# Performance work log

Measured on AMD Instinct MI355X. Metric: run time of the kernel, lower is better.

The kernel has to match this reference:

```python
import jax, jax.numpy as jnp
import numpy as np
from jax import lax

H = 64      # hidden_size
VOC = 512   # num_embedding
L = 2       # num_layers


def layernorm(x, g, b, eps=1e-5):
    mu = jnp.mean(x, axis=-1, keepdims=True)
    var = jnp.mean((x - mu) ** 2, axis=-1, keepdims=True)
    return (x - mu) * lax.rsqrt(var + eps) * g + b


def conv3d(x, w, b):
    # x: [B, U, V, W, Cin] (channels-last), w: [3,3,3,Cin,Cout]
    return lax.conv_general_dilated(
        x, w, (1, 1, 1), 'SAME',
        dimension_numbers=('NDHWC', 'DHWIO', 'NDHWC')) + b


def setup_inputs() -> dict:
    key = jax.random.key(0)
    ks = jax.random.split(key, 8)
    f = lambda k, s, sc: jax.random.normal(k, s, jnp.float32) * sc
    return {
        'code': jax.random.randint(ks[0], (2, 5, 1, 8, 8, 8), 0, VOC),
        'ncode': jax.random.randint(ks[1], (2, 3, 1, 8, 8, 8), 0, VOC),
        'emb': f(ks[2], (VOC, H), 0.02),
        'win': f(ks[3], (L, 3, 3, 3, H, 4 * H), 0.05),
        'bin_': jnp.zeros((L, 4 * H), jnp.float32),
        'gin_w': jnp.ones((L, 4 * H), jnp.float32),
        'gin_b': jnp.zeros((L, 4 * H), jnp.float32),
        'wh': f(ks[4], (L, 3, 3, 3, H, 4 * H), 0.05),
        'bh': jnp.zeros((L, 4 * H), jnp.float32),
        'gh_w': jnp.ones((L, 4 * H), jnp.float32),
        'gh_b': jnp.zeros((L, 4 * H), jnp.float32),
        'w1': f(ks[5], (H, H), 0.05),
        'b1': jnp.zeros((H,), jnp.float32),
        'ln_g': jnp.ones((H,), jnp.float32),
        'ln_b': jnp.zeros((H,), jnp.float32),
        'w2': f(ks[6], (H, VOC), 0.05),
        'b2': jnp.zeros((VOC,), jnp.float32),
    }


def _forward(code, ncode, emb, win, bin_, gin_w, gin_b, wh, bh, gh_w, gh_b,
             w1, b1, ln_g, ln_b, w2, b2):
    N, Sn, C, U, V, W = ncode.shape
    x = jnp.concatenate([code, ncode[:, :-1]], axis=1)  # [N,S,C,U,V,W]
    S = x.shape[1]
    x = jnp.transpose(x, (0, 2, 1, 3, 4, 5)).reshape(N * C, S, U, V, W)
    h = emb[x]  # [NC, S, U, V, W, H]
    Hd = h.shape[-1]
    for i in range(L):
        # input-path conv is recurrence-free: batch it over all timesteps
        gi = layernorm(conv3d(h.reshape(N * C * S, U, V, W, Hd), win[i], bin_[i]),
                       gin_w[i], gin_b[i])
        gi = jnp.moveaxis(gi.reshape(N * C, S, U, V, W, 4 * Hd), 1, 0)  # [S,NC,U,V,W,4H]

        def step(carry, g, i=i):
            hx, cx = carry
            gates = g + layernorm(conv3d(hx, wh[i], bh[i]), gh_w[i], gh_b[i])
            ig, fg, cg, og = jnp.split(gates, 4, axis=-1)
            cx = jax.nn.sigmoid(fg) * cx + jax.nn.sigmoid(ig) * jnp.tanh(cg)
            hx = jax.nn.sigmoid(og) * jnp.tanh(cx)
            return (hx, cx), hx

        z = jnp.zeros((N * C, U, V, W, Hd), h.dtype)
        _, ys = lax.scan(step, (z, z), gi)
        h = jnp.moveaxis(ys, 0, 1)  # [NC,S,U,V,W,H]
    h = h[:, -Sn:].reshape(N, C, Sn, U, V, W, Hd)
    h = jnp.transpose(h, (0, 2, 1, 3, 4, 5, 6))  # [N,Sn,C,U,V,W,H]
    z = jax.nn.gelu(layernorm(h @ w1 + b1, ln_g, ln_b), approximate=False)
    logits = z @ w2 + b2  # [N,Sn,C,U,V,W,VOC]
    score = jnp.transpose(logits, (0, 6, 1, 2, 3, 4, 5))  # [N,VOC,Sn,C,U,V,W]
    logp = jax.nn.log_softmax(logits, axis=-1)
    loss = -jnp.mean(jnp.take_along_axis(logp, ncode[..., None], axis=-1))
    pred = jnp.argmax(score, axis=1)
    return score, loss, pred


def reference(code, ncode, emb, win, bin_, gin_w, gin_b, wh, bh, gh_w, gh_b,
              w1, b1, ln_g, ln_b, w2, b2):
    return _forward(code, ncode, emb, win, bin_, gin_w, gin_b, wh, bh,
                    gh_w, gh_b, w1, b1, ln_g, ln_b, w2, b2)
```

## Files before the change

kernel.cpp:

```cpp
#include <hip/hip_runtime.h>


typedef _Float16 f16;
typedef _Float16 f16x8 __attribute__((ext_vector_type(8)));
typedef float    f32x4 __attribute__((ext_vector_type(4)));

#define WSTRIDE 442368
#define WPT     884736
#define XSP     65536
#define HSP     458752
#define GPART   262144

__device__ __forceinline__ float wred_sum(float v) {
    #pragma unroll
    for (int o = 32; o > 0; o >>= 1) v += __shfl_down(v, o, 64);
    return __shfl(v, 0, 64);
}
__device__ __forceinline__ float fsig(float x)  { return 1.f / (1.f + __expf(-x)); }
__device__ __forceinline__ float ftanh(float x) { return 1.f - 2.f / (__expf(2.f*x) + 1.f); }

__global__ __launch_bounds__(256) void prep_kernel(
    const int* __restrict__ code, const int* __restrict__ ncode,
    const float* __restrict__ emb, f16* __restrict__ h,
    const float* __restrict__ win, const float* __restrict__ wh,
    f16* __restrict__ wp)
{
    if (blockIdx.x < 1792) {
        int e = blockIdx.x * 256 + threadIdx.x;
        int ch = e & 63;
        int pos = e >> 6;
        int vox = pos & 511;
        int t = pos >> 9;
        int s = t % 7, nc = t / 7;
        int tok = (s < 5) ? code[(nc*5 + s)*512 + vox]
                          : ncode[(nc*3 + (s-5))*512 + vox];
        float x = emb[tok*64 + ch];
        f16 hi = (f16)x;
        h[(size_t)pos*128 + ch]      = hi;
        h[(size_t)pos*128 + 64 + ch] = (f16)(x - (float)hi);
    } else {
        int b = blockIdx.x - 1792;
        int tensor = b / 27, tap = b % 27;
        const float* src = ((tensor & 1) ? wh : win) + (tensor >> 1) * WSTRIDE
                         + tap * 16384;
        int co = threadIdx.x;
        int sw = co & 7;
        #pragma unroll
        for (int hs = 0; hs < 2; ++hs) {
            f16* dst = wp + (((size_t)tensor*27 + tap)*2 + hs)*16384 + co*64;
            #pragma unroll
            for (int j = 0; j < 4; ++j) {
                f16x8 hi8, lo8;
                #pragma unroll
                for (int m = 0; m < 8; ++m) {
                    float w = src[(hs*32 + j*8 + m)*256 + co] * 64.f;
                    f16 hv = (f16)w;
                    hi8[m] = hv;
                    lo8[m] = (f16)(w - (float)hv);
                }
                *(f16x8*)(dst + ((j     ^ sw))*8) = hi8;
                *(f16x8*)(dst + (((4+j) ^ sw))*8) = lo8;
            }
        }
    }
}

struct MJob { const f16* x; const f16* w; float* y; };
struct MJobs { MJob j[4]; };

__global__ __launch_bounds__(256, 3) void conv_mfma_kernel(MJobs js)
{
    const MJob J = js.j[blockIdx.y];
    __shared__ float4 smem[2048];
    f16* wbuf = (f16*)smem;

    const int bx = blockIdx.x;
    const int cog = bx & 3, u = (bx >> 2) & 7, slab = (bx >> 5) & 1;
    const int ah = (bx >> 6) & 1, kb = bx >> 7;
    const int t = threadIdx.x, wid = t >> 6, l = t & 63;
    const int lv = (l >> 3) & 1, lw = l & 7, khi = l >> 4;

    const int gid = kb*4 + wid;
    const int g0  = (gid < 6) ? gid*7 : 42 + (gid - 6)*6;
    const int cnt = (gid < 6) ? 7 : 6;

    const f16* xbase = J.x + (size_t)slab * HSP;
    const f16* wjob  = J.w + (size_t)cog * 4096;
    f16* wmine = wbuf + wid * 4096;

    f16x8 wreg[8];
    auto wload = [&](int k) {
        const f16* src = wjob + (size_t)k * 16384 + l * 8;
        #pragma unroll
        for (int i = 0; i < 8; ++i) wreg[i] = *(const f16x8*)(src + i * 512);
    };
    auto wstore = [&]() {
        f16* dst = wmine + l * 8;
        #pragma unroll
        for (int i = 0; i < 8; ++i) *(f16x8*)(dst + i * 512) = wreg[i];
    };

    wload(g0); wstore();

    f32x4 acc[2][4] = {};
    for (int q = 0; q < cnt; ++q) {
        const int k = g0 + q;
        if (q + 1 < cnt) wload(k + 1);
        const int tap = k >> 1, hs = k & 1;
        const int du = tap / 9, rr = tap % 9, dv = rr / 3, dw = rr % 3;
        const int uu = u + du - 1;
        const bool uok = (unsigned)uu < 8u;
        const f16* xrow[2]; bool ok[2];
        #pragma unroll
        for (int aa = 0; aa < 2; ++aa) {
            int vs = (ah*2 + aa)*2 + lv + dv - 1, ws = lw + dw - 1;
            ok[aa] = uok && (unsigned)vs < 8u && (unsigned)ws < 8u;
            xrow[aa] = xbase + ((size_t)(uu*64 + vs*8 + ws) << 7) + khi*8;
        }
        const f16* wrow = wmine + (l & 15)*64;
        const int schi = ((khi    ) ^ lw) * 8;
        const int sclo = ((4 + khi) ^ lw) * 8;
        f16x8 ahi[2], alo[2], bhi[4], blo[4];
        #pragma unroll
        for (int aa = 0; aa < 2; ++aa) {
            f16x8 v = {0,0,0,0,0,0,0,0}, v2 = v;
            if (ok[aa]) {
                v  = *(const f16x8*)(xrow[aa] + hs*32);
                v2 = *(const f16x8*)(xrow[aa] + 64 + hs*32);
            }
            ahi[aa] = v; alo[aa] = v2;
        }
        #pragma unroll
        for (int n = 0; n < 4; ++n) {
            bhi[n] = *(const f16x8*)(wrow + n*1024 + schi);
            blo[n] = *(const f16x8*)(wrow + n*1024 + sclo);
        }
        #pragma unroll
        for (int aa = 0; aa < 2; ++aa)
            #pragma unroll
            for (int n = 0; n < 4; ++n)
                acc[aa][n] = __builtin_amdgcn_mfma_f32_16x16x32_f16(
                    ahi[aa], bhi[n], acc[aa][n], 0, 0, 0);
        #pragma unroll
        for (int aa = 0; aa < 2; ++aa)
            #pragma unroll
            for (int n = 0; n < 4; ++n)
                acc[aa][n] = __builtin_amdgcn_mfma_f32_16x16x32_f16(
                    alo[aa], bhi[n], acc[aa][n], 0, 0, 0);
        #pragma unroll
        for (int aa = 0; aa < 2; ++aa)
            #pragma unroll
            for (int n = 0; n < 4; ++n)
                acc[aa][n] = __builtin_amdgcn_mfma_f32_16x16x32_f16(
                    ahi[aa], blo[n], acc[aa][n], 0, 0, 0);
        if (q + 1 < cnt) wstore();
    }

    f32x4* red = (f32x4*)smem;
    {
        f32x4* mine = red + (size_t)(wid * 64 + l) * 8;
        #pragma unroll
        for (int aa = 0; aa < 2; ++aa)
            #pragma unroll
            for (int n = 0; n < 4; ++n)
                mine[(aa * 4 + n) ^ lw] = acc[aa][n];
    }
    __syncthreads();
    {
        float* yp = J.y + (size_t)kb * GPART;
        const int aa = (t >> 7) & 1, nsel = (t >> 6) & 1, ll = t & 63;
        #pragma unroll
        for (int ni = 0; ni < 2; ++ni) {
            const int n = nsel*2 + ni;
            const int ch = (aa * 4 + n) ^ (ll & 7);
            f32x4 sv = red[(0 * 64 + ll) * 8 + ch]
                     + red[(1 * 64 + ll) * 8 + ch]
                     + red[(2 * 64 + ll) * 8 + ch]
                     + red[(3 * 64 + ll) * 8 + ch];
            const int co = cog * 64 + n * 16 + (ll & 15);
            #pragma unroll
            for (int r = 0; r < 4; ++r) {
                int vox = (ah*2 + aa) * 16 + (ll >> 4) * 4 + r;
                yp[(size_t)(slab * 512 + u * 64 + vox) * 256 + co]
                    = sv[r] * 0.015625f;
            }
        }
    }
}

struct GJob {
    const float* giA; const float* giB;
    const float* ghA; const float* ghB;
    const float* bin; const float* bhb;
    const float* ginw; const float* ginb;
    const float* ghw;  const float* ghb;
    float* cx; f16* h16; int k; int k0;
};
__global__ __launch_bounds__(256) void gates_step_kernel(GJob ja, GJob jb)
{
    const GJob J = (blockIdx.y == 0) ? ja : jb;
    const int wid = threadIdx.x >> 6, lane = threadIdx.x & 63;
    const int row = blockIdx.x * 4 + wid;
    const int nc = row >> 9, vox = row & 511;

    const float* gA = J.giA + (size_t)row*256;
    const float* gB = J.giB + (size_t)row*256;
    float a0 = gA[lane]     + gB[lane]     + J.bin[lane];
    float a1 = gA[64+lane]  + gB[64+lane]  + J.bin[64+lane];
    float a2 = gA[128+lane] + gB[128+lane] + J.bin[128+lane];
    float a3 = gA[192+lane] + gB[192+lane] + J.bin[192+lane];
    float mu1 = wred_sum(a0+a1+a2+a3) * (1.f/256.f);
    float d0=a0-mu1, d1=a1-mu1, d2=a2-mu1, d3=a3-mu1;
    float v1 = wred_sum(d0*d0+d1*d1+d2*d2+d3*d3) * (1.f/256.f);
    float rs1 = rsqrtf(v1 + 1e-5f);

    float b0, b1, b2, b3;
    if (J.k0) {
        b0 = J.bhb[lane]; b1 = J.bhb[64+lane];
        b2 = J.bhb[128+lane]; b3 = J.bhb[192+lane];
    } else {
        const float* hA = J.ghA + (size_t)row*256;
        const float* hB = J.ghB + (size_t)row*256;
        b0 = hA[lane]     + hB[lane]     + J.bhb[lane];
        b1 = hA[64+lane]  + hB[64+lane]  + J.bhb[64+lane];
        b2 = hA[128+lane] + hB[128+lane] + J.bhb[128+lane];
        b3 = hA[192+lane] + hB[192+lane] + J.bhb[192+lane];
    }
    float mu2 = wred_sum(b0+b1+b2+b3) * (1.f/256.f);
    float e0=b0-mu2, e1=b1-mu2, e2=b2-mu2, e3=b3-mu2;
    float v2 = wred_sum(e0*e0+e1*e1+e2*e2+e3*e3) * (1.f/256.f);
    float rs2 = rsqrtf(v2 + 1e-5f);

    float Ig = d0*rs1*J.ginw[lane]     + J.ginb[lane]     + e0*rs2*J.ghw[lane]     + J.ghb[lane];
    float Fg = d1*rs1*J.ginw[64+lane]  + J.ginb[64+lane]  + e1*rs2*J.ghw[64+lane]  + J.ghb[64+lane];
    float Cg = d2*rs1*J.ginw[128+lane] + J.ginb[128+lane] + e2*rs2*J.ghw[128+lane] + J.ghb[128+lane];
    float Og = d3*rs1*J.ginw[192+lane] + J.ginb[192+lane] + e3*rs2*J.ghw[192+lane] + J.ghb[192+lane];

    float c_old = J.k0 ? 0.f : J.cx[(size_t)row*64 + lane];
    float c_new = fsig(Fg)*c_old + fsig(Ig)*ftanh(Cg);
    float h_new = fsig(Og)*ftanh(c_new);
    J.cx[(size_t)row*64 + lane] = c_new;
    size_t hb = ((size_t)(nc*7 + J.k)*512 + vox)*128 + lane;
    f16 hi = (f16)h_new;
    J.h16[hb]      = hi;
    J.h16[hb + 64] = (f16)(h_new - (float)hi);
}

__global__ __launch_bounds__(256) void head_kernel(
    const f16* __restrict__ h,
    const float* __restrict__ w1, const float* __restrict__ b1,
    const float* __restrict__ lng, const float* __restrict__ lnb,
    const float* __restrict__ w2, const float* __restrict__ b2,
    const int* __restrict__ ncode,
    float* __restrict__ out)
{
    __shared__ float hsm[16][64];
    __shared__ float zv[16][64];
    __shared__ float lg[10240];
    __shared__ float lsum[16];
    const int blk = blockIdx.x;
    const int n = blk / 96;
    const int sn = (blk / 32) % 3;
    const int vox0 = (blk & 31) * 16;
    const int t = threadIdx.x, wid = t >> 6, lane = t & 63;

    for (int idx = t; idx < 1024; idx += 256) {
        int vr = idx >> 6, ch = idx & 63;
        const f16* hv = h + (size_t)((n*7 + sn + 4)*512 + vox0 + vr)*128;
        hsm[vr][ch] = (float)hv[ch] + (float)hv[64 + ch];
    }
    __syncthreads();

    float yva[4], yvb[4];
    #pragma unroll
    for (int r = 0; r < 4; ++r) { yva[r] = b1[lane]; yvb[r] = 0.f; }
    for (int kk = 0; kk < 64; kk += 2) {
        float w1a = w1[kk*64 + lane], w1b = w1[(kk+1)*64 + lane];
        #pragma unroll
        for (int r = 0; r < 4; ++r) {
            yva[r] = fmaf(hsm[wid*4 + r][kk],     w1a, yva[r]);
            yvb[r] = fmaf(hsm[wid*4 + r][kk + 1], w1b, yvb[r]);
        }
    }
    #pragma unroll
    for (int r = 0; r < 4; ++r) {
        float yv = yva[r] + yvb[r];
        float mu = wred_sum(yv) * (1.f/64.f);
        float d = yv - mu;
        float var = wred_sum(d*d) * (1.f/64.f);
        float ln = d * rsqrtf(var + 1e-5f) * lng[lane] + lnb[lane];
        zv[wid*4 + r][lane] = 0.5f * ln * (1.f + erff(ln * 0.70710678118654752f));
    }
    __syncthreads();

    float l[4][8];
    #pragma unroll
    for (int r = 0; r < 4; ++r)
        #pragma unroll
        for (int j = 0; j < 8; ++j) l[r][j] = b2[j*64 + lane];
    for (int kk = 0; kk < 64; ++kk) {
        float wv[8];
        #pragma unroll
        for (int j = 0; j < 8; ++j) wv[j] = w2[kk*512 + j*64 + lane];
        #pragma unroll
        for (int r = 0; r < 4; ++r) {
            float zz = zv[wid*4 + r][kk];
            #pragma unroll
            for (int j = 0; j < 8; ++j) l[r][j] = fmaf(zz, wv[j], l[r][j]);
        }
    }
    #pragma unroll
    for (int r = 0; r < 4; ++r)
        #pragma unroll
        for (int j = 0; j < 8; ++j)
            lg[(j*64 + lane)*20 + wid*4 + r] = l[r][j];

    #pragma unroll
    for (int r = 0; r < 4; ++r) {
        float m = l[r][0]; int mi = lane;
        #pragma unroll
        for (int j = 1; j < 8; ++j)
            if (l[r][j] > m) { m = l[r][j]; mi = j*64 + lane; }
        #pragma unroll
        for (int o = 32; o > 0; o >>= 1) {
            float om = __shfl_down(m, o, 64);
            int   oi = __shfl_down(mi, o, 64);
            if (om > m || (om == m && oi < mi)) { m = om; mi = oi; }
        }
        float maxv = __shfl(m, 0, 64);
        int   maxi = __shfl(mi, 0, 64);
        float es = 0.f;
        #pragma unroll
        for (int j = 0; j < 8; ++j) es += __expf(l[r][j] - maxv);
        float sum = wred_sum(es);
        if (lane == 0) {
            int vox = vox0 + wid*4 + r;
            int target = ncode[(n*3 + sn)*512 + vox];
            float logp = lg[target*20 + wid*4 + r] - maxv - __logf(sum);
            lsum[wid*4 + r] = -logp * (1.f/3072.f);
            out[1572865 + (n*3 + sn)*512 + vox] = (float)maxi;
        }
    }

    __syncthreads();
    if (t == 0) {
        float s = 0.f;
        #pragma unroll
        for (int i = 0; i < 16; ++i) s += lsum[i];
        atomicAdd(out + 1572864, s);
    }
    for (int e = t; e < 2048; e += 256) {
        int co = e >> 2, p = e & 3;
        int base = co*20 + p*4;
        float4 o4 = { lg[base], lg[base+1], lg[base+2], lg[base+3] };
        *(float4*)(out + (size_t)((n*512 + co)*3 + sn)*512 + vox0 + p*4) = o4;
    }
}

extern "C" void kernel_launch(void* const* d_in, const int* in_sizes, int n_in,
                              void* d_out, int out_size, void* d_ws, size_t ws_size,
                              hipStream_t stream) {
    (void)in_sizes; (void)n_in; (void)out_size; (void)ws_size;
    const int*   code  = (const int*)d_in[0];
    const int*   ncode = (const int*)d_in[1];
    const float* emb   = (const float*)d_in[2];
    const float* win   = (const float*)d_in[3];
    const float* bin_  = (const float*)d_in[4];
    const float* gin_w = (const float*)d_in[5];
    const float* gin_b = (const float*)d_in[6];
    const float* wh    = (const float*)d_in[7];
    const float* bh    = (const float*)d_in[8];
    const float* gh_w  = (const float*)d_in[9];
    const float* gh_b  = (const float*)d_in[10];
    const float* w1    = (const float*)d_in[11];
    const float* b1    = (const float*)d_in[12];
    const float* ln_g  = (const float*)d_in[13];
    const float* ln_b  = (const float*)d_in[14];
    const float* w2    = (const float*)d_in[15];
    const float* b2    = (const float*)d_in[16];
    float* out = (float*)d_out;

    float* base  = (float*)d_ws;
    f16*   wp    = (f16*)base;
    f16*   h1    = (f16*)(base + 1769472);
    f16*   h2    = h1 + 917504;
    float* gi1   = base + 2686976;
    float* gi2   = gi1 + 2*GPART;
    float* ghat1 = gi2 + 2*GPART;
    float* ghat2 = ghat1 + 2*GPART;
    float* cx1   = ghat2 + 2*GPART;
    float* cx2   = cx1 + 65536;

    const f16* win0 = wp;
    const f16* wh0  = wp + WPT;
    const f16* win1 = wp + 2*WPT;
    const f16* wh1  = wp + 3*WPT;

    hipMemsetAsync(out + 1572864, 0, sizeof(float), stream);
    prep_kernel<<<1900, 256, 0, stream>>>(code, ncode, emb, h1, win, wh, wp);

    {
        MJobs js{};
        js.j[0] = { h1, win0, gi1 };
        conv_mfma_kernel<<<dim3(256, 1), 256, 0, stream>>>(js);
    }

    for (int s = 0; s <= 7; ++s) {
        GJob g1 = { gi1, gi1 + GPART, ghat1, ghat1 + GPART, bin_, bh,
                    gin_w, gin_b, gh_w, gh_b, cx1, h1, s, s == 0 };
        GJob g2 = { gi2, gi2 + GPART, ghat2, ghat2 + GPART, bin_ + 256, bh + 256,
                    gin_w + 256, gin_b + 256, gh_w + 256, gh_b + 256,
                    cx2, h2, s - 1, s == 1 };
        if (s == 0)
            gates_step_kernel<<<dim3(256, 1), 256, 0, stream>>>(g1, g1);
        else if (s <= 6)
            gates_step_kernel<<<dim3(256, 2), 256, 0, stream>>>(g1, g2);
        else
            gates_step_kernel<<<dim3(256, 1), 256, 0, stream>>>(g2, g2);

        MJobs js{}; int nj = 0;
        if (s <= 5) js.j[nj++] = { h1 + (size_t)(s+1)*XSP, win0, gi1 };
        if (s <= 5) js.j[nj++] = { h1 + (size_t)s*XSP,     wh0,  ghat1 };
        if (s <= 6) js.j[nj++] = { h1 + (size_t)s*XSP,     win1, gi2 };
        if (s >= 1 && s <= 6)
                    js.j[nj++] = { h2 + (size_t)(s-1)*XSP, wh1,  ghat2 };
        if (nj > 0)
            conv_mfma_kernel<<<dim3(256, nj), 256, 0, stream>>>(js);
    }

    head_kernel<<<192, 256, 0, stream>>>(h2, w1, b1, ln_g, ln_b, w2, b2, ncode, out);
}
```

Measured before the change: 305.0 us.

## Fuse the LSTM timestep loop into a persistent cooperative megakernel with grid syncs

Replaces the separate prep, conv and gates kernel launches per timestep with one cooperative persistent kernel. The stages are separated by grid-wide barriers, and each block works through the tiles with a grid-stride loop. It also hoists the layer-0 input convolution for all seven timesteps into one batched phase up front, which enlarges the gi1 workspace. The aim is to remove per-launch overhead and to fill the GPU better. In exchange it adds grid-sync costs, depends on cooperative-launch occupancy, and needs a bigger workspace.

New measurement: 868.5 us. +184.7%, slower.

```diff
diff --git a/kernel.cpp b/kernel.cpp
--- a/kernel.cpp
+++ b/kernel.cpp
@@ -1,4 +1,6 @@
 #include <hip/hip_runtime.h>
+#include <hip/hip_cooperative_groups.h>
+namespace cg = cooperative_groups;
 
 
 typedef _Float16 f16;
@@ -19,35 +21,51 @@
 __device__ __forceinline__ float fsig(float x)  { return 1.f / (1.f + __expf(-x)); }
 __device__ __forceinline__ float ftanh(float x) { return 1.f - 2.f / (__expf(2.f*x) + 1.f); }
 
-__global__ __launch_bounds__(256) void prep_kernel(
-    const int* __restrict__ code, const int* __restrict__ ncode,
-    const float* __restrict__ emb, f16* __restrict__ h,
-    const float* __restrict__ win, const float* __restrict__ wh,
-    f16* __restrict__ wp)
-{
-    if (blockIdx.x < 1792) {
-        int e = blockIdx.x * 256 + threadIdx.x;
+struct MJob { const f16* x; const f16* w; float* y; };
+struct GJob {
+    const float* giA; const float* giB;
+    const float* ghA; const float* ghB;
+    const float* bin; const float* bhb;
+    const float* ginw; const float* ginb;
+    const float* ghw;  const float* ghb;
+    float* cx; f16* h16; int k; int k0;
+};
+struct MegaArgs {
+    const int* code; const int* ncode; const float* emb;
+    const float* win; const float* wh;
+    const float* bin_; const float* bh;
+    const float* gin_w; const float* gin_b;
+    const float* gh_w;  const float* gh_b;
+    f16* wp; f16* h1; f16* h2;
+    float* gi1; float* gi2; float* ghat1; float* ghat2;
+    float* cx1; float* cx2;
+};
+
+
+__device__ void prep_task(const MegaArgs& A, int task, int t) {
+    if (task < 1792) {
+        int e = task * 256 + t;
         int ch = e & 63;
         int pos = e >> 6;
         int vox = pos & 511;
-        int t = pos >> 9;
-        int s = t % 7, nc = t / 7;
-        int tok = (s < 5) ? code[(nc*5 + s)*512 + vox]
-                          : ncode[(nc*3 + (s-5))*512 + vox];
-        float x = emb[tok*64 + ch];
+        int tt = pos >> 9;
+        int s = tt % 7, nc = tt / 7;
+        int tok = (s < 5) ? A.code[(nc*5 + s)*512 + vox]
+                          : A.ncode[(nc*3 + (s-5))*512 + vox];
+        float x = A.emb[tok*64 + ch];
         f16 hi = (f16)x;
-        h[(size_t)pos*128 + ch]      = hi;
-        h[(size_t)pos*128 + 64 + ch] = (f16)(x - (float)hi);
+        A.h1[(size_t)pos*128 + ch]      = hi;
+        A.h1[(size_t)pos*128 + 64 + ch] = (f16)(x - (float)hi);
     } else {
-        int b = blockIdx.x - 1792;
+        int b = task - 1792;
         int tensor = b / 27, tap = b % 27;
-        const float* src = ((tensor & 1) ? wh : win) + (tensor >> 1) * WSTRIDE
-                         + tap * 16384;
-        int co = threadIdx.x;
+        const float* src = ((tensor & 1) ? A.wh : A.win)
+                         + (tensor >> 1) * WSTRIDE + tap * 16384;
+        int co = t;
         int sw = co & 7;
         #pragma unroll
         for (int hs = 0; hs < 2; ++hs) {
-            f16* dst = wp + (((size_t)tensor*27 + tap)*2 + hs)*16384 + co*64;
+            f16* dst = A.wp + (((size_t)tensor*27 + tap)*2 + hs)*16384 + co*64;
             #pragma unroll
             for (int j = 0; j < 4; ++j) {
                 f16x8 hi8, lo8;
@@ -65,19 +83,11 @@
     }
 }
 
-struct MJob { const f16* x; const f16* w; float* y; };
-struct MJobs { MJob j[4]; };
-
-__global__ __launch_bounds__(256, 3) void conv_mfma_kernel(MJobs js)
-{
-    const MJob J = js.j[blockIdx.y];
-    __shared__ float4 smem[2048];
+__device__ void conv_tile(const MJob& J, int bx, int t, float4* smem) {
     f16* wbuf = (f16*)smem;
-
-    const int bx = blockIdx.x;
     const int cog = bx & 3, u = (bx >> 2) & 7, slab = (bx >> 5) & 1;
     const int ah = (bx >> 6) & 1, kb = bx >> 7;
-    const int t = threadIdx.x, wid = t >> 6, l = t & 63;
+    const int wid = t >> 6, l = t & 63;
     const int lv = (l >> 3) & 1, lw = l & 7, khi = l >> 4;
 
     const int gid = kb*4 + wid;
@@ -186,21 +196,12 @@
             }
         }
     }
-}
-
-struct GJob {
-    const float* giA; const float* giB;
-    const float* ghA; const float* ghB;
-    const float* bin; const float* bhb;
-    const float* ginw; const float* ginb;
-    const float* ghw;  const float* ghb;
-    float* cx; f16* h16; int k; int k0;
-};
-__global__ __launch_bounds__(256) void gates_step_kernel(GJob ja, GJob jb)
-{
-    const GJob J = (blockIdx.y == 0) ? ja : jb;
-    const int wid = threadIdx.x >> 6, lane = threadIdx.x & 63;
-    const int row = blockIdx.x * 4 + wid;
+    __syncthreads();
+}
+
+__device__ void gates_task(const GJob& J, int bx, int t) {
+    const int wid = t >> 6, lane = t & 63;
+    const int row = bx * 4 + wid;
     const int nc = row >> 9, vox = row & 511;
 
     const float* gA = J.giA + (size_t)row*256;
@@ -244,6 +245,67 @@
     f16 hi = (f16)h_new;
     J.h16[hb]      = hi;
     J.h16[hb + 64] = (f16)(h_new - (float)hi);
+}
+
+__global__ __launch_bounds__(256, 3) void mega_kernel(MegaArgs A)
+{
+    cg::grid_group gg = cg::this_grid();
+    __shared__ float4 smem[2048];
+    const int nb = gridDim.x, bid = blockIdx.x, t = threadIdx.x;
+    const f16* win0 = A.wp;
+    const f16* wh0  = A.wp + WPT;
+    const f16* win1 = A.wp + 2*WPT;
+    const f16* wh1  = A.wp + 3*WPT;
+
+    for (int task = bid; task < 1900; task += nb) prep_task(A, task, t);
+    gg.sync();
+
+    for (int task = bid; task < 1792; task += nb) {
+        int s = task >> 8;
+        MJob m = { A.h1 + (size_t)s*XSP, win0, A.gi1 + (size_t)s*2*GPART };
+        conv_tile(m, task & 255, t, smem);
+    }
+    gg.sync();
+
+    for (int s = 0; s <= 7; ++s) {
+        GJob gj0, gj1; int ngj = 0;
+        if (s <= 6) {
+            gj0 = { A.gi1 + (size_t)s*2*GPART, A.gi1 + (size_t)s*2*GPART + GPART,
+                    A.ghat1, A.ghat1 + GPART, A.bin_, A.bh,
+                    A.gin_w, A.gin_b, A.gh_w, A.gh_b, A.cx1, A.h1, s, s == 0 };
+            ngj = 1;
+        }
+        if (s >= 1) {
+            GJob g2 = { A.gi2, A.gi2 + GPART, A.ghat2, A.ghat2 + GPART,
+                        A.bin_ + 256, A.bh + 256, A.gin_w + 256, A.gin_b + 256,
+                        A.gh_w + 256, A.gh_b + 256, A.cx2, A.h2, s - 1, s == 1 };
+            if (ngj == 0) gj0 = g2; else gj1 = g2;
+            ++ngj;
+        }
+        for (int task = bid; task < ngj*256; task += nb)
+            gates_task((task >> 8) ? gj1 : gj0, task & 255, t);
+        gg.sync();
+
+        MJob cj0{}, cj1{}, cj2{}; int ncj = 0;
+        if (s <= 5) { cj0 = { A.h1 + (size_t)s*XSP, wh0, A.ghat1 }; ncj = 1; }
+        if (s <= 6) {
+            MJob m = { A.h1 + (size_t)s*XSP, win1, A.gi2 };
+            if (ncj == 0) cj0 = m; else cj1 = m;
+            ++ncj;
+        }
+        if (s >= 1 && s <= 6) {
+            MJob m = { A.h2 + (size_t)(s-1)*XSP, wh1, A.ghat2 };
+            if (ncj == 0) cj0 = m; else if (ncj == 1) cj1 = m; else cj2 = m;
+            ++ncj;
+        }
+        if (ncj) {
+            for (int task = bid; task < ncj*256; task += nb) {
+                int q = task >> 8;
+                conv_tile(q == 0 ? cj0 : (q == 1 ? cj1 : cj2), task & 255, t, smem);
+            }
+            gg.sync();
+        }
+    }
 }
 
 __global__ __launch_bounds__(256) void head_kernel(
@@ -383,50 +445,31 @@
     float* base  = (float*)d_ws;
     f16*   wp    = (f16*)base;
     f16*   h1    = (f16*)(base + 1769472);
-    f16*   h2    = h1 + 917504;
+    f16*   h2    = (f16*)(base + 2228224);
     float* gi1   = base + 2686976;
-    float* gi2   = gi1 + 2*GPART;
+    float* gi2   = gi1 + 7*2*GPART;
     float* ghat1 = gi2 + 2*GPART;
     float* ghat2 = ghat1 + 2*GPART;
     float* cx1   = ghat2 + 2*GPART;
     float* cx2   = cx1 + 65536;
 
-    const f16* win0 = wp;
-    const f16* wh0  = wp + WPT;
-    const f16* win1 = wp + 2*WPT;
-    const f16* wh1  = wp + 3*WPT;
+    MegaArgs A = { code, ncode, emb, win, wh, bin_, bh,
+                   gin_w, gin_b, gh_w, gh_b,
+                   wp, h1, h2, gi1, gi2, ghat1, ghat2, cx1, cx2 };
 
     hipMemsetAsync(out + 1572864, 0, sizeof(float), stream);
-    prep_kernel<<<1900, 256, 0, stream>>>(code, ncode, emb, h1, win, wh, wp);
-
-    {
-        MJobs js{};
-        js.j[0] = { h1, win0, gi1 };
-        conv_mfma_kernel<<<dim3(256, 1), 256, 0, stream>>>(js);
-    }
-
-    for (int s = 0; s <= 7; ++s) {
-        GJob g1 = { gi1, gi1 + GPART, ghat1, ghat1 + GPART, bin_, bh,
-                    gin_w, gin_b, gh_w, gh_b, cx1, h1, s, s == 0 };
-        GJob g2 = { gi2, gi2 + GPART, ghat2, ghat2 + GPART, bin_ + 256, bh + 256,
-                    gin_w + 256, gin_b + 256, gh_w + 256, gh_b + 256,
-                    cx2, h2, s - 1, s == 1 };
-        if (s == 0)
-            gates_step_kernel<<<dim3(256, 1), 256, 0, stream>>>(g1, g1);
-        else if (s <= 6)
-            gates_step_kernel<<<dim3(256, 2), 256, 0, stream>>>(g1, g2);
-        else
-            gates_step_kernel<<<dim3(256, 1), 256, 0, stream>>>(g2, g2);
-
-        MJobs js{}; int nj = 0;
-        if (s <= 5) js.j[nj++] = { h1 + (size_t)(s+1)*XSP, win0, gi1 };
-        if (s <= 5) js.j[nj++] = { h1 + (size_t)s*XSP,     wh0,  ghat1 };
-        if (s <= 6) js.j[nj++] = { h1 + (size_t)s*XSP,     win1, gi2 };
-        if (s >= 1 && s <= 6)
-                    js.j[nj++] = { h2 + (size_t)(s-1)*XSP, wh1,  ghat2 };
-        if (nj > 0)
-            conv_mfma_kernel<<<dim3(256, nj), 256, 0, stream>>>(js);
-    }
+
+    static int nblk = 0;
+    if (nblk == 0) {
+        int occ = 0;
+        if (hipOccupancyMaxActiveBlocksPerMultiprocessor(&occ, mega_kernel, 256, 0)
+                != hipSuccess || occ < 1)
+            occ = 1;
+        nblk = occ * 256;
+        if (nblk > 768) nblk = 768;
+    }
+    void* kargs[] = { (void*)&A };
+    hipLaunchCooperativeKernel(mega_kernel, dim3(nblk), dim3(256), kargs, 0, stream);
 
     head_kernel<<<192, 256, 0, stream>>>(h2, w1, b1, ln_g, ln_b, w2, b2, ncode, out);
 }
```

## Batch layer-0 input conv over all timesteps and use four-way K split

Applied to the files above, without the earlier changes.

The layer-0 input-path convolution for all seven timesteps now runs as one up-front launch writing per-timestep partial buffers, so it leaves the recurrent per-step conv launches. The conv kernel now covers all four voxel row-groups per block (acc 4x4) and splits the 54 K-chunks into four partial sums instead of two. The gates kernel sums four partials. This shortens the serial critical path and raises per-block reuse, at the cost of more registers (launch bounds drop to 2 blocks per SM), more workspace, and extra partial-sum reads.

Result: slower. 319.6 us (+4.8%).

```diff
diff --git a/kernel.cpp b/kernel.cpp
--- a/kernel.cpp
+++ b/kernel.cpp
@@ -66,23 +66,22 @@
 }
 
 struct MJob { const f16* x; const f16* w; float* y; };
-struct MJobs { MJob j[4]; };
-
-__global__ __launch_bounds__(256, 3) void conv_mfma_kernel(MJobs js)
+struct MJobs { MJob j[8]; };
+
+__global__ __launch_bounds__(256, 2) void conv_mfma_kernel(MJobs js)
 {
     const MJob J = js.j[blockIdx.y];
     __shared__ float4 smem[2048];
     f16* wbuf = (f16*)smem;
 
     const int bx = blockIdx.x;
-    const int cog = bx & 3, u = (bx >> 2) & 7, slab = (bx >> 5) & 1;
-    const int ah = (bx >> 6) & 1, kb = bx >> 7;
+    const int cog = bx & 3, u = (bx >> 2) & 7, slab = (bx >> 5) & 1, kb = bx >> 6;
     const int t = threadIdx.x, wid = t >> 6, l = t & 63;
     const int lv = (l >> 3) & 1, lw = l & 7, khi = l >> 4;
 
     const int gid = kb*4 + wid;
-    const int g0  = (gid < 6) ? gid*7 : 42 + (gid - 6)*6;
-    const int cnt = (gid < 6) ? 7 : 6;
+    const int g0  = (gid < 6) ? gid*4 : 24 + (gid - 6)*3;
+    const int cnt = (gid < 6) ? 4 : 3;
 
     const f16* xbase = J.x + (size_t)slab * HSP;
     const f16* wjob  = J.w + (size_t)cog * 4096;
@@ -102,7 +101,7 @@
 
     wload(g0); wstore();
 
-    f32x4 acc[2][4] = {};
+    f32x4 acc[4][4] = {};
     for (int q = 0; q < cnt; ++q) {
         const int k = g0 + q;
         if (q + 1 < cnt) wload(k + 1);
@@ -110,25 +109,25 @@
         const int du = tap / 9, rr = tap % 9, dv = rr / 3, dw = rr % 3;
         const int uu = u + du - 1;
         const bool uok = (unsigned)uu < 8u;
-        const f16* xrow[2]; bool ok[2];
-        #pragma unroll
-        for (int aa = 0; aa < 2; ++aa) {
-            int vs = (ah*2 + aa)*2 + lv + dv - 1, ws = lw + dw - 1;
-            ok[aa] = uok && (unsigned)vs < 8u && (unsigned)ws < 8u;
-            xrow[aa] = xbase + ((size_t)(uu*64 + vs*8 + ws) << 7) + khi*8;
+        const f16* xrow[4]; bool ok[4];
+        #pragma unroll
+        for (int a = 0; a < 4; ++a) {
+            int vs = a*2 + lv + dv - 1, ws = lw + dw - 1;
+            ok[a] = uok && (unsigned)vs < 8u && (unsigned)ws < 8u;
+            xrow[a] = xbase + ((size_t)(uu*64 + vs*8 + ws) << 7) + khi*8;
         }
         const f16* wrow = wmine + (l & 15)*64;
         const int schi = ((khi    ) ^ lw) * 8;
         const int sclo = ((4 + khi) ^ lw) * 8;
-        f16x8 ahi[2], alo[2], bhi[4], blo[4];
-        #pragma unroll
-        for (int aa = 0; aa < 2; ++aa) {
+        f16x8 ahi[4], alo[4], bhi[4], blo[4];
+        #pragma unroll
+        for (int a = 0; a < 4; ++a) {
             f16x8 v = {0,0,0,0,0,0,0,0}, v2 = v;
-            if (ok[aa]) {
-                v  = *(const f16x8*)(xrow[aa] + hs*32);
-                v2 = *(const f16x8*)(xrow[aa] + 64 + hs*32);
+            if (ok[a]) {
+                v  = *(const f16x8*)(xrow[a] + hs*32);
+                v2 = *(const f16x8*)(xrow[a] + 64 + hs*32);
             }
-            ahi[aa] = v; alo[aa] = v2;
+            ahi[a] = v; alo[a] = v2;
         }
         #pragma unroll
         for (int n = 0; n < 4; ++n) {
@@ -136,61 +135,65 @@
             blo[n] = *(const f16x8*)(wrow + n*1024 + sclo);
         }
         #pragma unroll
-        for (int aa = 0; aa < 2; ++aa)
+        for (int a = 0; a < 4; ++a)
             #pragma unroll
             for (int n = 0; n < 4; ++n)
-                acc[aa][n] = __builtin_amdgcn_mfma_f32_16x16x32_f16(
-                    ahi[aa], bhi[n], acc[aa][n], 0, 0, 0);
-        #pragma unroll
-        for (int aa = 0; aa < 2; ++aa)
+                acc[a][n] = __builtin_amdgcn_mfma_f32_16x16x32_f16(
+                    ahi[a], bhi[n], acc[a][n], 0, 0, 0);
+        #pragma unroll
+        for (int a = 0; a < 4; ++a)
             #pragma unroll
             for (int n = 0; n < 4; ++n)
-                acc[aa][n] = __builtin_amdgcn_mfma_f32_16x16x32_f16(
-                    alo[aa], bhi[n], acc[aa][n], 0, 0, 0);
-        #pragma unroll
-        for (int aa = 0; aa < 2; ++aa)
+                acc[a][n] = __builtin_amdgcn_mfma_f32_16x16x32_f16(
+                    alo[a], bhi[n], acc[a][n], 0, 0, 0);
+        #pragma unroll
+        for (int a = 0; a < 4; ++a)
             #pragma unroll
             for (int n = 0; n < 4; ++n)
-                acc[aa][n] = __builtin_amdgcn_mfma_f32_16x16x32_f16(
-                    ahi[aa], blo[n], acc[aa][n], 0, 0, 0);
+                acc[a][n] = __builtin_amdgcn_mfma_f32_16x16x32_f16(
+                    ahi[a], blo[n], acc[a][n], 0, 0, 0);
         if (q + 1 < cnt) wstore();
     }
 
     f32x4* red = (f32x4*)smem;
-    {
-        f32x4* mine = red + (size_t)(wid * 64 + l) * 8;
-        #pragma unroll
-        for (int aa = 0; aa < 2; ++aa)
-            #pragma unroll
-            for (int n = 0; n < 4; ++n)
-                mine[(aa * 4 + n) ^ lw] = acc[aa][n];
-    }
-    __syncthreads();
-    {
-        float* yp = J.y + (size_t)kb * GPART;
-        const int aa = (t >> 7) & 1, nsel = (t >> 6) & 1, ll = t & 63;
-        #pragma unroll
-        for (int ni = 0; ni < 2; ++ni) {
-            const int n = nsel*2 + ni;
-            const int ch = (aa * 4 + n) ^ (ll & 7);
-            f32x4 sv = red[(0 * 64 + ll) * 8 + ch]
-                     + red[(1 * 64 + ll) * 8 + ch]
-                     + red[(2 * 64 + ll) * 8 + ch]
-                     + red[(3 * 64 + ll) * 8 + ch];
-            const int co = cog * 64 + n * 16 + (ll & 15);
-            #pragma unroll
-            for (int r = 0; r < 4; ++r) {
-                int vox = (ah*2 + aa) * 16 + (ll >> 4) * 4 + r;
-                yp[(size_t)(slab * 512 + u * 64 + vox) * 256 + co]
-                    = sv[r] * 0.015625f;
+    float* yp = J.y + (size_t)kb * GPART;
+    #pragma unroll
+    for (int half = 0; half < 2; ++half) {
+        {
+            f32x4* mine = red + (size_t)(wid * 64 + l) * 8;
+            #pragma unroll
+            for (int aa = 0; aa < 2; ++aa)
+                #pragma unroll
+                for (int n = 0; n < 4; ++n)
+                    mine[(aa * 4 + n) ^ lw] = acc[half*2 + aa][n];
+        }
+        __syncthreads();
+        {
+            const int aa = (t >> 7) & 1, nsel = (t >> 6) & 1, ll = t & 63;
+            #pragma unroll
+            for (int ni = 0; ni < 2; ++ni) {
+                const int n = nsel*2 + ni;
+                const int ch = (aa * 4 + n) ^ (ll & 7);
+                f32x4 sv = red[(0 * 64 + ll) * 8 + ch]
+                         + red[(1 * 64 + ll) * 8 + ch]
+                         + red[(2 * 64 + ll) * 8 + ch]
+                         + red[(3 * 64 + ll) * 8 + ch];
+                const int co = cog * 64 + n * 16 + (ll & 15);
+                #pragma unroll
+                for (int r = 0; r < 4; ++r) {
+                    int vox = (half*2 + aa) * 16 + (ll >> 4) * 4 + r;
+                    yp[(size_t)(slab * 512 + u * 64 + vox) * 256 + co]
+                        = sv[r] * 0.015625f;
+                }
             }
         }
+        __syncthreads();
     }
 }
 
 struct GJob {
-    const float* giA; const float* giB;
-    const float* ghA; const float* ghB;
+    const float* gi;
+    const float* gh;
     const float* bin; const float* bhb;
     const float* ginw; const float* ginb;
     const float* ghw;  const float* ghb;
@@ -203,12 +206,20 @@
     const int row = blockIdx.x * 4 + wid;
     const int nc = row >> 9, vox = row & 511;
 
-    const float* gA = J.giA + (size_t)row*256;
-    const float* gB = J.giB + (size_t)row*256;
-    float a0 = gA[lane]     + gB[lane]     + J.bin[lane];
-    float a1 = gA[64+lane]  + gB[64+lane]  + J.bin[64+lane];
-    float a2 = gA[128+lane] + gB[128+lane] + J.bin[128+lane];
-    float a3 = gA[192+lane] + gB[192+lane] + J.bin[192+lane];
+    const float* g = J.gi + (size_t)row*256;
+    float a0, a1, a2, a3;
+    {
+        float s0 = g[lane]             + g[GPART+lane]
+                 + g[2*GPART+lane]     + g[3*GPART+lane];
+        float s1 = g[64+lane]          + g[GPART+64+lane]
+                 + g[2*GPART+64+lane]  + g[3*GPART+64+lane];
+        float s2 = g[128+lane]         + g[GPART+128+lane]
+                 + g[2*GPART+128+lane] + g[3*GPART+128+lane];
+        float s3 = g[192+lane]         + g[GPART+192+lane]
+                 + g[2*GPART+192+lane] + g[3*GPART+192+lane];
+        a0 = s0 + J.bin[lane];       a1 = s1 + J.bin[64+lane];
+        a2 = s2 + J.bin[128+lane];   a3 = s3 + J.bin[192+lane];
+    }
     float mu1 = wred_sum(a0+a1+a2+a3) * (1.f/256.f);
     float d0=a0-mu1, d1=a1-mu1, d2=a2-mu1, d3=a3-mu1;
     float v1 = wred_sum(d0*d0+d1*d1+d2*d2+d3*d3) * (1.f/256.f);
@@ -219,12 +230,15 @@
         b0 = J.bhb[lane]; b1 = J.bhb[64+lane];
         b2 = J.bhb[128+lane]; b3 = J.bhb[192+lane];
     } else {
-        const float* hA = J.ghA + (size_t)row*256;
-        const float* hB = J.ghB + (size_t)row*256;
-        b0 = hA[lane]     + hB[lane]     + J.bhb[lane];
-        b1 = hA[64+lane]  + hB[64+lane]  + J.bhb[64+lane];
-        b2 = hA[128+lane] + hB[128+lane] + J.bhb[128+lane];
-        b3 = hA[192+lane] + hB[192+lane] + J.bhb[192+lane];
+        const float* hh = J.gh + (size_t)row*256;
+        b0 = hh[lane]             + hh[GPART+lane]
+           + hh[2*GPART+lane]     + hh[3*GPART+lane]     + J.bhb[lane];
+        b1 = hh[64+lane]          + hh[GPART+64+lane]
+           + hh[2*GPART+64+lane]  + hh[3*GPART+64+lane]  + J.bhb[64+lane];
+        b2 = hh[128+lane]         + hh[GPART+128+lane]
+           + hh[2*GPART+128+lane] + hh[3*GPART+128+lane] + J.bhb[128+lane];
+        b3 = hh[192+lane]         + hh[GPART+192+lane]
+           + hh[2*GPART+192+lane] + hh[3*GPART+192+lane] + J.bhb[192+lane];
     }
     float mu2 = wred_sum(b0+b1+b2+b3) * (1.f/256.f);
     float e0=b0-mu2, e1=b1-mu2, e2=b2-mu2, e3=b3-mu2;
@@ -383,12 +397,12 @@
     float* base  = (float*)d_ws;
     f16*   wp    = (f16*)base;
     f16*   h1    = (f16*)(base + 1769472);
-    f16*   h2    = h1 + 917504;
+    f16*   h2    = (f16*)(base + 2228224);
     float* gi1   = base + 2686976;
-    float* gi2   = gi1 + 2*GPART;
-    float* ghat1 = gi2 + 2*GPART;
-    float* ghat2 = ghat1 + 2*GPART;
-    float* cx1   = ghat2 + 2*GPART;
+    float* gi2   = gi1 + 7*4*(size_t)GPART;
+    float* ghat1 = gi2 + 4*(size_t)GPART;
+    float* ghat2 = ghat1 + 4*(size_t)GPART;
+    float* cx1   = ghat2 + 4*(size_t)GPART;
     float* cx2   = cx1 + 65536;
 
     const f16* win0 = wp;
@@ -401,14 +415,15 @@
 
     {
         MJobs js{};
-        js.j[0] = { h1, win0, gi1 };
-        conv_mfma_kernel<<<dim3(256, 1), 256, 0, stream>>>(js);
+        for (int s = 0; s < 7; ++s)
+            js.j[s] = { h1 + (size_t)s*XSP, win0, gi1 + (size_t)s*4*GPART };
+        conv_mfma_kernel<<<dim3(256, 7), 256, 0, stream>>>(js);
     }
 
     for (int s = 0; s <= 7; ++s) {
-        GJob g1 = { gi1, gi1 + GPART, ghat1, ghat1 + GPART, bin_, bh,
+        GJob g1 = { gi1 + (size_t)s*4*GPART, ghat1, bin_, bh,
                     gin_w, gin_b, gh_w, gh_b, cx1, h1, s, s == 0 };
-        GJob g2 = { gi2, gi2 + GPART, ghat2, ghat2 + GPART, bin_ + 256, bh + 256,
+        GJob g2 = { gi2, ghat2, bin_ + 256, bh + 256,
                     gin_w + 256, gin_b + 256, gh_w + 256, gh_b + 256,
                     cx2, h2, s - 1, s == 1 };
         if (s == 0)
@@ -419,7 +434,6 @@
             gates_step_kernel<<<dim3(256, 1), 256, 0, stream>>>(g2, g2);
 
         MJobs js{}; int nj = 0;
-        if (s <= 5) js.j[nj++] = { h1 + (size_t)(s+1)*XSP, win0, gi1 };
         if (s <= 5) js.j[nj++] = { h1 + (size_t)s*XSP,     wh0,  ghat1 };
         if (s <= 6) js.j[nj++] = { h1 + (size_t)s*XSP,     win1, gi2 };
         if (s >= 1 && s <= 6)
```

## Batch layer-0 input convolutions upfront and split head across more blocks

Applied to the files above, without the earlier changes.

The layer-0 input-path convolution has no recurrence, so all 7 timesteps are now computed in one launch before the scan. Each timestep gets its own gi1 slice in a larger workspace, which drops one conv job from every per-step launch on the critical path. The head kernel now handles 4 voxels per block (768 blocks) instead of 16, to raise parallelism, at the cost of more repeated w1/w2 reads across blocks. The loss atomicAdd and memset are replaced by per-block partial sums plus a small deterministic final reduction kernel.

Result: no change. 305.7 us (+0.2%).

```diff
diff --git a/kernel.cpp b/kernel.cpp
--- a/kernel.cpp
+++ b/kernel.cpp
@@ -66,7 +66,7 @@
 }
 
 struct MJob { const f16* x; const f16* w; float* y; };
-struct MJobs { MJob j[4]; };
+struct MJobs { MJob j[8]; };
 
 __global__ __launch_bounds__(256, 3) void conv_mfma_kernel(MJobs js)
 {
@@ -252,109 +252,84 @@
     const float* __restrict__ lng, const float* __restrict__ lnb,
     const float* __restrict__ w2, const float* __restrict__ b2,
     const int* __restrict__ ncode,
-    float* __restrict__ out)
+    float* __restrict__ out, float* __restrict__ lossb)
 {
-    __shared__ float hsm[16][64];
-    __shared__ float zv[16][64];
-    __shared__ float lg[10240];
-    __shared__ float lsum[16];
+    __shared__ float hsm[4][64];
+    __shared__ float zv[4][64];
+    __shared__ float lg[4][512];
+    __shared__ float lsum[4];
     const int blk = blockIdx.x;
-    const int n = blk / 96;
-    const int sn = (blk / 32) % 3;
-    const int vox0 = (blk & 31) * 16;
+    const int n = blk / 384;
+    const int sn = (blk / 128) % 3;
+    const int vox0 = (blk & 127) * 4;
     const int t = threadIdx.x, wid = t >> 6, lane = t & 63;
-
-    for (int idx = t; idx < 1024; idx += 256) {
-        int vr = idx >> 6, ch = idx & 63;
-        const f16* hv = h + (size_t)((n*7 + sn + 4)*512 + vox0 + vr)*128;
-        hsm[vr][ch] = (float)hv[ch] + (float)hv[64 + ch];
-    }
+    const int vox = vox0 + wid;
+    const f16* hv = h + (size_t)((n*7 + sn + 4)*512 + vox)*128;
+
+    hsm[wid][lane] = (float)hv[lane] + (float)hv[64 + lane];
+
+    float yva = b1[lane], yvb = 0.f;
+    for (int kk = 0; kk < 64; kk += 2) {
+        yva = fmaf(hsm[wid][kk],     w1[kk*64 + lane],     yva);
+        yvb = fmaf(hsm[wid][kk + 1], w1[(kk+1)*64 + lane], yvb);
+    }
+    float yv = yva + yvb;
+    float mu = wred_sum(yv) * (1.f/64.f);
+    float d = yv - mu;
+    float var = wred_sum(d*d) * (1.f/64.f);
+    float ln = d * rsqrtf(var + 1e-5f) * lng[lane] + lnb[lane];
+    zv[wid][lane] = 0.5f * ln * (1.f + erff(ln * 0.70710678118654752f));
+
+    float l[8];
+    #pragma unroll
+    for (int j = 0; j < 8; ++j) l[j] = b2[j*64 + lane];
+    for (int kk = 0; kk < 64; ++kk) {
+        float zz = zv[wid][kk];
+        #pragma unroll
+        for (int j = 0; j < 8; ++j)
+            l[j] = fmaf(zz, w2[kk*512 + j*64 + lane], l[j]);
+    }
+    #pragma unroll
+    for (int j = 0; j < 8; ++j) lg[wid][j*64 + lane] = l[j];
+
+    float m = l[0]; int mi = lane;
+    #pragma unroll
+    for (int j = 1; j < 8; ++j)
+        if (l[j] > m) { m = l[j]; mi = j*64 + lane; }
+    #pragma unroll
+    for (int o = 32; o > 0; o >>= 1) {
+        float om = __shfl_down(m, o, 64);
+        int   oi = __shfl_down(mi, o, 64);
+        if (om > m || (om == m && oi < mi)) { m = om; mi = oi; }
+    }
+    float maxv = __shfl(m, 0, 64);
+    int   maxi = __shfl(mi, 0, 64);
+    float es = 0.f;
+    #pragma unroll
+    for (int j = 0; j < 8; ++j) es += __expf(l[j] - maxv);
+    float sum = wred_sum(es);
+    if (lane == 0) {
+        int target = ncode[(n*3 + sn)*512 + vox];
+        float logp = lg[wid][target] - maxv - __logf(sum);
+        lsum[wid] = -logp * (1.f/3072.f);
+        out[1572865 + (n*3 + sn)*512 + vox] = (float)maxi;
+    }
+
     __syncthreads();
-
-    float yva[4], yvb[4];
-    #pragma unroll
-    for (int r = 0; r < 4; ++r) { yva[r] = b1[lane]; yvb[r] = 0.f; }
-    for (int kk = 0; kk < 64; kk += 2) {
-        float w1a = w1[kk*64 + lane], w1b = w1[(kk+1)*64 + lane];
-        #pragma unroll
-        for (int r = 0; r < 4; ++r) {
-            yva[r] = fmaf(hsm[wid*4 + r][kk],     w1a, yva[r]);
-            yvb[r] = fmaf(hsm[wid*4 + r][kk + 1], w1b, yvb[r]);
-        }
-    }
-    #pragma unroll
-    for (int r = 0; r < 4; ++r) {
-        float yv = yva[r] + yvb[r];
-        float mu = wred_sum(yv) * (1.f/64.f);
-        float d = yv - mu;
-        float var = wred_sum(d*d) * (1.f/64.f);
-        float ln = d * rsqrtf(var + 1e-5f) * lng[lane] + lnb[lane];
-        zv[wid*4 + r][lane] = 0.5f * ln * (1.f + erff(ln * 0.70710678118654752f));
-    }
-    __syncthreads();
-
-    float l[4][8];
-    #pragma unroll
-    for (int r = 0; r < 4; ++r)
-        #pragma unroll
-        for (int j = 0; j < 8; ++j) l[r][j] = b2[j*64 + lane];
-    for (int kk = 0; kk < 64; ++kk) {
-        float wv[8];
-        #pragma unroll
-        for (int j = 0; j < 8; ++j) wv[j] = w2[kk*512 + j*64 + lane];
-        #pragma unroll
-        for (int r = 0; r < 4; ++r) {
-            float zz = zv[wid*4 + r][kk];
-            #pragma unroll
-            for (int j = 0; j < 8; ++j) l[r][j] = fmaf(zz, wv[j], l[r][j]);
-        }
-    }
-    #pragma unroll
-    for (int r = 0; r < 4; ++r)
-        #pragma unroll
-        for (int j = 0; j < 8; ++j)
-            lg[(j*64 + lane)*20 + wid*4 + r] = l[r][j];
-
-    #pragma unroll
-    for (int r = 0; r < 4; ++r) {
-        float m = l[r][0]; int mi = lane;
-        #pragma unroll
-        for (int j = 1; j < 8; ++j)
-            if (l[r][j] > m) { m = l[r][j]; mi = j*64 + lane; }
-        #pragma unroll
-        for (int o = 32; o > 0; o >>= 1) {
-            float om = __shfl_down(m, o, 64);
-            int   oi = __shfl_down(mi, o, 64);
-            if (om > m || (om == m && oi < mi)) { m = om; mi = oi; }
-        }
-        float maxv = __shfl(m, 0, 64);
-        int   maxi = __shfl(mi, 0, 64);
-        float es = 0.f;
-        #pragma unroll
-        for (int j = 0; j < 8; ++j) es += __expf(l[r][j] - maxv);
-        float sum = wred_sum(es);
-        if (lane == 0) {
-            int vox = vox0 + wid*4 + r;
-            int target = ncode[(n*3 + sn)*512 + vox];
-            float logp = lg[target*20 + wid*4 + r] - maxv - __logf(sum);
-            lsum[wid*4 + r] = -logp * (1.f/3072.f);
-            out[1572865 + (n*3 + sn)*512 + vox] = (float)maxi;
-        }
-    }
-
-    __syncthreads();
-    if (t == 0) {
-        float s = 0.f;
-        #pragma unroll
-        for (int i = 0; i < 16; ++i) s += lsum[i];
-        atomicAdd(out + 1572864, s);
-    }
-    for (int e = t; e < 2048; e += 256) {
-        int co = e >> 2, p = e & 3;
-        int base = co*20 + p*4;
-        float4 o4 = { lg[base], lg[base+1], lg[base+2], lg[base+3] };
-        *(float4*)(out + (size_t)((n*512 + co)*3 + sn)*512 + vox0 + p*4) = o4;
-    }
+    if (t == 0) lossb[blk] = lsum[0] + lsum[1] + lsum[2] + lsum[3];
+    for (int co = t; co < 512; co += 256) {
+        float4 o4 = { lg[0][co], lg[1][co], lg[2][co], lg[3][co] };
+        *(float4*)(out + (size_t)((n*512 + co)*3 + sn)*512 + vox0) = o4;
+    }
+}
+
+__global__ void loss_fin_kernel(const float* __restrict__ lossb,
+                                float* __restrict__ out)
+{
+    float s = 0.f;
+    for (int i = threadIdx.x; i < 768; i += 64) s += lossb[i];
+    s = wred_sum(s);
+    if (threadIdx.x == 0) out[1572864] = s;
 }
 
 extern "C" void kernel_launch(void* const* d_in, const int* in_sizes, int n_in,
@@ -383,30 +358,32 @@
     float* base  = (float*)d_ws;
     f16*   wp    = (f16*)base;
     f16*   h1    = (f16*)(base + 1769472);
-    f16*   h2    = h1 + 917504;
+    f16*   h2    = (f16*)(base + 2228224);
     float* gi1   = base + 2686976;
-    float* gi2   = gi1 + 2*GPART;
+    float* gi2   = gi1 + 7*2*(size_t)GPART;
     float* ghat1 = gi2 + 2*GPART;
     float* ghat2 = ghat1 + 2*GPART;
     float* cx1   = ghat2 + 2*GPART;
     float* cx2   = cx1 + 65536;
+    float* lossb = base + 8060928;
 
     const f16* win0 = wp;
     const f16* wh0  = wp + WPT;
     const f16* win1 = wp + 2*WPT;
     const f16* wh1  = wp + 3*WPT;
 
-    hipMemsetAsync(out + 1572864, 0, sizeof(float), stream);
     prep_kernel<<<1900, 256, 0, stream>>>(code, ncode, emb, h1, win, wh, wp);
 
     {
         MJobs js{};
-        js.j[0] = { h1, win0, gi1 };
-        conv_mfma_kernel<<<dim3(256, 1), 256, 0, stream>>>(js);
+        for (int s = 0; s < 7; ++s)
+            js.j[s] = { h1 + (size_t)s*XSP, win0, gi1 + (size_t)s*2*GPART };
+        conv_mfma_kernel<<<dim3(256, 7), 256, 0, stream>>>(js);
     }
 
     for (int s = 0; s <= 7; ++s) {
-        GJob g1 = { gi1, gi1 + GPART, ghat1, ghat1 + GPART, bin_, bh,
+        GJob g1 = { gi1 + (size_t)s*2*GPART, gi1 + (size_t)s*2*GPART + GPART,
+                    ghat1, ghat1 + GPART, bin_, bh,
                     gin_w, gin_b, gh_w, gh_b, cx1, h1, s, s == 0 };
         GJob g2 = { gi2, gi2 + GPART, ghat2, ghat2 + GPART, bin_ + 256, bh + 256,
                     gin_w + 256, gin_b + 256, gh_w + 256, gh_b + 256,
@@ -419,7 +396,6 @@
             gates_step_kernel<<<dim3(256, 1), 256, 0, stream>>>(g2, g2);
 
         MJobs js{}; int nj = 0;
-        if (s <= 5) js.j[nj++] = { h1 + (size_t)(s+1)*XSP, win0, gi1 };
         if (s <= 5) js.j[nj++] = { h1 + (size_t)s*XSP,     wh0,  ghat1 };
         if (s <= 6) js.j[nj++] = { h1 + (size_t)s*XSP,     win1, gi2 };
         if (s >= 1 && s <= 6)
@@ -428,5 +404,7 @@
             conv_mfma_kernel<<<dim3(256, nj), 256, 0, stream>>>(js);
     }
 
-    head_kernel<<<192, 256, 0, stream>>>(h2, w1, b1, ln_g, ln_b, w2, b2, ncode, out);
-}
+    head_kernel<<<768, 256, 0, stream>>>(h2, w1, b1, ln_g, ln_b, w2, b2,
+                                         ncode, out, lossb);
+    loss_fin_kernel<<<1, 64, 0, stream>>>(lossb, out);
+}
```
